# Performance work log

Hardware: AMD Instinct MI355X
Metric: run time of the kernel (lower is better)

The kernel has to match this reference:

```python
import jax, jax.numpy as jnp
import numpy as np

B, S, D, E, H, TOPK = 4, 2048, 1024, 32, 128, 4

def setup_inputs() -> dict:
    key = jax.random.key(0)
    k1, k2, k3, k4 = jax.random.split(key, 4)
    x = jax.random.normal(k1, (B, S, D), jnp.float32)
    expert_sel = jax.random.normal(k2, (E, D), jnp.float32) * (D ** -0.5)
    keys = jax.random.normal(k3, (E, D, H), jnp.float32) * (D ** -0.5)
    values = jax.random.normal(k4, (E, H, D), jnp.float32) * (H ** -0.5)
    return {"x": x, "expert_sel": expert_sel, "keys": keys, "values": values, "n_heads": TOPK}

def reference(x, expert_sel, keys, values, n_heads):
    # x: [B,S,D]; expert_sel: [E,D]; keys: [E,D,H]; values: [E,H,D]
    Bv, Sv, Dv = x.shape
    Ev = keys.shape[0]
    xf = x.reshape(-1, Dv)                                  # [N,D]
    N = xf.shape[0]
    gate = jax.nn.sigmoid(xf @ expert_sel.T)                # [N,E] sigmoid gating (sigma-MoE)
    vals, idx = jax.lax.top_k(gate, n_heads)                # [N,k] selected experts + gate weights
    # dense per-token-per-expert gate weights; zero for non-selected experts
    g = jnp.zeros((N, Ev), x.dtype).at[jnp.arange(N)[:, None], idx].set(vals)  # [N,E]
    # grouped expert FFN, expressed densely over the (small) expert axis:
    # out = sum_e g[n,e] * relu(x @ keys[e]) @ values[e]
    h = jax.nn.relu(jnp.einsum('nd,edh->enh', xf, keys))    # [E,N,H]
    out = jnp.einsum('enh,ehd->nd', h * g.T[:, :, None], values)  # [N,D]
    return out.reshape(Bv, Sv, Dv)
```

## Files before the change

kernel.cpp:

```cpp
#include <hip/hip_runtime.h>
#include <hip/hip_bf16.h>

#define NTOK 8192
#define DDIM 1024
#define NEXP 32
#define HDIM 128
#define TOPK 4

typedef __attribute__((ext_vector_type(8))) short bf16x8;
typedef __attribute__((ext_vector_type(4))) float f32x4;

typedef unsigned int uint_g __attribute__((address_space(1)));
typedef unsigned int uint_l __attribute__((address_space(3)));

__device__ __forceinline__ void async_cp16(const void* g, void* l) {
    __builtin_amdgcn_global_load_lds((const uint_g*)g, (uint_l*)l, 16, 0, 0);
}

__device__ inline unsigned short f2bf(float f) {
    unsigned int u = __builtin_bit_cast(unsigned int, f);
    unsigned int r = (u + 0x7fffu + ((u >> 16) & 1u)) >> 16;
    return (unsigned short)r;
}
__device__ inline float bf2f(unsigned short s) {
    unsigned int u = ((unsigned int)s) << 16;
    return __builtin_bit_cast(float, u);
}

__global__ __launch_bounds__(256) void prep_gate(
    const float* __restrict__ x, const float* __restrict__ es,
    const float* __restrict__ keys, const float* __restrict__ values,
    unsigned short* __restrict__ Kb, unsigned short* __restrict__ Vb,
    unsigned short* __restrict__ Xb,
    int* __restrict__ cnt, int* __restrict__ tok_list, float* __restrict__ gates)
{
    const int tid = threadIdx.x;

    if (blockIdx.x >= 512) {
        int idx = (int)(blockIdx.x - 512) * 256 + tid;
        unsigned short o[8];
        if (idx < NEXP * 128 * 128) {
            int n = idx & 127, k0 = (idx >> 7) & 127, e = idx >> 14;
            const float* s = keys + ((size_t)e * DDIM + k0 * 8) * HDIM + n;
            #pragma unroll
            for (int j = 0; j < 8; ++j) o[j] = f2bf(s[(size_t)j * HDIM]);
            *(uint4*)&Kb[(size_t)idx * 8] = *(uint4*)o;
        } else {
            idx -= NEXP * 128 * 128;
            int n = idx & 1023, k0 = (idx >> 10) & 15, e = idx >> 14;
            const float* s = values + ((size_t)e * HDIM + k0 * 8) * DDIM + n;
            #pragma unroll
            for (int j = 0; j < 8; ++j) o[j] = f2bf(s[(size_t)j * DDIM]);
            *(uint4*)&Vb[(size_t)idx * 8] = *(uint4*)o;
        }
        return;
    }

    const int n0 = (int)blockIdx.x * 16;

    __shared__ float smem[4608];
    __shared__ float Ls[16 * 33];
    __shared__ int hist[NEXP];
    __shared__ int bbase[NEXP];
    float* Xt  = smem;
    float* Est = smem + 64 * 36;
    float* Lp  = smem;

    const int t4  = (tid & 3) * 4;
    const int e4  = ((tid >> 2) & 7) * 4;
    const int rep = tid >> 5;

    const int xr = tid & 15, xc4 = (tid >> 4) * 4;
    const int er = tid & 31, ec8 = (tid >> 5) * 8;

    const int ctok = tid >> 4, cd4 = (tid & 15) * 4;

    const int rtok = tid >> 5, re = tid & 31;

    float lsum[2] = {0.f, 0.f};

    if (tid < NEXP) hist[tid] = 0;

    float4 xv  = *(const float4*)&x[(size_t)(n0 + xr) * DDIM + xc4];
    float4 ev0 = *(const float4*)&es[(size_t)er * DDIM + ec8];
    float4 ev1 = *(const float4*)&es[(size_t)er * DDIM + ec8 + 4];

    for (int q = 0; q < 4; ++q) {
        float acc[4][4] = {};

        for (int dci = 0; dci < 4; ++dci) {
            const int dc = q * 256 + dci * 64;
            __syncthreads();
            {
                Xt[(xc4 + 0) * 36 + xr] = xv.x; Xt[(xc4 + 1) * 36 + xr] = xv.y;
                Xt[(xc4 + 2) * 36 + xr] = xv.z; Xt[(xc4 + 3) * 36 + xr] = xv.w;
                Est[(ec8 + 0) * 36 + er] = ev0.x; Est[(ec8 + 1) * 36 + er] = ev0.y;
                Est[(ec8 + 2) * 36 + er] = ev0.z; Est[(ec8 + 3) * 36 + er] = ev0.w;
                Est[(ec8 + 4) * 36 + er] = ev1.x; Est[(ec8 + 5) * 36 + er] = ev1.y;
                Est[(ec8 + 6) * 36 + er] = ev1.z; Est[(ec8 + 7) * 36 + er] = ev1.w;
            }
            const int nxt = dc + 64;
            if (nxt < DDIM) {
                xv  = *(const float4*)&x[(size_t)(n0 + xr) * DDIM + nxt + xc4];
                ev0 = *(const float4*)&es[(size_t)er * DDIM + nxt + ec8];
                ev1 = *(const float4*)&es[(size_t)er * DDIM + nxt + ec8 + 4];
            }
            __syncthreads();

            {
                unsigned short o[4];
                #pragma unroll
                for (int j = 0; j < 4; ++j) o[j] = f2bf(Xt[(cd4 + j) * 36 + ctok]);
                *(uint2*)&Xb[(size_t)(n0 + ctok) * DDIM + dc + cd4] = *(uint2*)o;
            }

            #pragma unroll
            for (int s = 0; s < 8; ++s) {
                int d = s * 8 + rep;
                float4 xa4 = *(const float4*)&Xt[d * 36 + t4];
                float4 ea4 = *(const float4*)&Est[d * 36 + e4];
                const float xa[4] = {xa4.x, xa4.y, xa4.z, xa4.w};
                const float ea[4] = {ea4.x, ea4.y, ea4.z, ea4.w};
                #pragma unroll
                for (int i = 0; i < 4; ++i)
                    #pragma unroll
                    for (int j = 0; j < 4; ++j)
                        acc[i][j] = fmaf(xa[i], ea[j], acc[i][j]);
            }
        }

        __syncthreads();
        #pragma unroll
        for (int i = 0; i < 4; ++i)
            #pragma unroll
            for (int j = 0; j < 4; ++j)
                Lp[(rep * 16 + t4 + i) * 33 + e4 + j] = acc[i][j];
        __syncthreads();

        #pragma unroll
        for (int h = 0; h < 2; ++h) {
            int tok = rtok + h * 8;
            float s = 0.f;
            #pragma unroll
            for (int r = 0; r < 8; ++r) s += Lp[(r * 16 + tok) * 33 + re];
            lsum[h] += s;
        }
    }

    #pragma unroll
    for (int h = 0; h < 2; ++h) Ls[(rtok + h * 8) * 33 + re] = lsum[h];
    __syncthreads();

    int sel[TOPK]; int lpos[TOPK];
    if (tid < 16) {
        float lg[NEXP];
        #pragma unroll
        for (int e2 = 0; e2 < NEXP; ++e2) lg[e2] = Ls[tid * 33 + e2];
        float sv[TOPK];
        #pragma unroll
        for (int j = 0; j < TOPK; ++j) {
            float bv = -3.0e38f; int bi = 0;
            #pragma unroll
            for (int e2 = 0; e2 < NEXP; ++e2) {
                bool taken = false;
                #pragma unroll
                for (int qq = 0; qq < j; ++qq) taken = taken || (sel[qq] == e2);
                float v = taken ? -3.0e38f : lg[e2];
                if (v > bv) { bv = v; bi = e2; }
            }
            sel[j] = bi; sv[j] = bv;
        }
        #pragma unroll
        for (int j = 0; j < TOPK; ++j) {
            gates[(size_t)(n0 + tid) * TOPK + j] = 1.f / (1.f + expf(-sv[j]));
            lpos[j] = atomicAdd(&hist[sel[j]], 1);
        }
    }
    __syncthreads();
    if (tid < NEXP) bbase[tid] = atomicAdd(&cnt[tid], hist[tid]);
    __syncthreads();
    if (tid < 16) {
        #pragma unroll
        for (int j = 0; j < TOPK; ++j)
            tok_list[(size_t)sel[j] * NTOK + bbase[sel[j]] + lpos[j]] = (n0 + tid) * TOPK + j;
    }
}

__global__ __launch_bounds__(256) void ffn_fused(
    const unsigned short* __restrict__ Xb,
    const unsigned short* __restrict__ Kb,
    const unsigned short* __restrict__ Vb,
    const int* __restrict__ cnt, const int* __restrict__ tok_list,
    const float* __restrict__ gates,
    unsigned short* __restrict__ Ob)
{
    const int bid = blockIdx.x;
    const int e = bid & 31, tile = bid >> 5;
    const int c = cnt[e], base = tile * 64;
    if (base >= c) return;
    const int nt   = min(64, c - base);
    const int tid  = threadIdx.x, wave = tid >> 6, lane = tid & 63;
    const int lm   = lane & 15, quad = lane >> 4;
    const int r2   = (wave >> 1) * 32;
    const int c2   = (wave & 1) * 64;
    const int cw   = (wave & 1) * 32;

    __shared__ __align__(16) unsigned short KV[8192];
    __shared__ __align__(16) unsigned short XO[4608];
    __shared__ __align__(16) unsigned short Hs[64 * 140];
    __shared__ int slot[64]; __shared__ int gtok[64]; __shared__ float gs[64];

    if (tid < 64) {
        if (tid < nt) {
            int v = tok_list[(size_t)e * NTOK + base + tid];
            slot[tid] = v; gtok[tid] = v >> 2; gs[tid] = gates[v];
        } else { slot[tid] = -1; gtok[tid] = 0; gs[tid] = 0.f; }
    }
    __syncthreads();

    const unsigned short* Ke = Kb + (size_t)e * 131072;
    const unsigned short* Ve = Vb + (size_t)e * 131072;

    f32x4 acc[2][4];
    #pragma unroll
    for (int i = 0; i < 2; ++i)
        #pragma unroll
        for (int j = 0; j < 4; ++j) acc[i][j] = (f32x4){0.f, 0.f, 0.f, 0.f};

    const int xrow = (lane >> 3);
    const int xsub = (lane & 7);
    auto stageA = [&](int t) {
        int dc = t * 64;
        #pragma unroll
        for (int i = 0; i < 4; ++i) {
            int p = wave * 4 + i;
            async_cp16(Ke + ((size_t)(dc / 8 + (p >> 1)) * 128 + (p & 1) * 64 + lane) * 8,
                       &KV[p * 512]);
        }
        #pragma unroll
        for (int i = 0; i < 2; ++i) {
            int j = wave * 2 + i;
            int row = j * 8 + xrow;
            int u = xsub ^ (row & 7);
            async_cp16(Xb + (size_t)gtok[row] * DDIM + dc + u * 8, &XO[j * 512]);
        }
    };

    stageA(0);
    __syncthreads();

    const int xx = (quad << 3);
    for (int t = 0; t < 16; ++t) {
        #pragma unroll
        for (int ks = 0; ks < 2; ++ks) {
            int k0 = ks * 4 + quad;
            int xo = ((k0 ^ (lm & 7)) & 7) * 8;
            bf16x8 a0 = *(const bf16x8*)&XO[(r2 + lm) * 64 + xo];
            bf16x8 a1 = *(const bf16x8*)&XO[(r2 + 16 + lm) * 64 + xo];
            #pragma unroll
            for (int tj = 0; tj < 4; ++tj) {
                bf16x8 bb = *(const bf16x8*)&KV[(k0 * 128 + c2 + tj * 16 + lm) * 8];
                acc[0][tj] = __builtin_amdgcn_mfma_f32_16x16x32_bf16(a0, bb, acc[0][tj], 0, 0, 0);
                acc[1][tj] = __builtin_amdgcn_mfma_f32_16x16x32_bf16(a1, bb, acc[1][tj], 0, 0, 0);
            }
        }
        if (t < 15) {
            __syncthreads();
            stageA(t + 1);
            __syncthreads();
        }
    }
    (void)xx;

    #pragma unroll
    for (int ti = 0; ti < 2; ++ti)
        #pragma unroll
        for (int reg = 0; reg < 4; ++reg) {
            int m = r2 + ti * 16 + quad * 4 + reg;
            float g = gs[m];
            #pragma unroll
            for (int tj = 0; tj < 4; ++tj)
                Hs[m * 140 + c2 + tj * 16 + lm] = f2bf(fmaxf(acc[ti][tj][reg], 0.f) * g);
        }
    __syncthreads();

    auto stageV = [&](int cc) {
        #pragma unroll
        for (int i = 0; i < 4; ++i) {
            int p = wave * 4 + i;
            async_cp16(Ve + ((size_t)p * 1024 + cc * 64 + lane) * 8, &KV[p * 512]);
        }
    };

    stageV(0);

    bf16x8 hf[2][4];
    #pragma unroll
    for (int ks = 0; ks < 4; ++ks) {
        hf[0][ks] = *(const bf16x8*)&Hs[(r2 + lm) * 140 + (ks * 4 + quad) * 8];
        hf[1][ks] = *(const bf16x8*)&Hs[(r2 + 16 + lm) * 140 + (ks * 4 + quad) * 8];
    }
    __syncthreads();

    const int om = tid >> 2, oq = tid & 3;
    const int os = slot[om];

    for (int cc = 0; cc < 16; ++cc) {
        f32x4 acc2[2][2];
        #pragma unroll
        for (int i = 0; i < 2; ++i) {
            acc2[i][0] = (f32x4){0.f, 0.f, 0.f, 0.f};
            acc2[i][1] = (f32x4){0.f, 0.f, 0.f, 0.f};
        }

        #pragma unroll
        for (int ks = 0; ks < 4; ++ks) {
            int k0 = ks * 4 + quad;
            #pragma unroll
            for (int tj = 0; tj < 2; ++tj) {
                bf16x8 bb = *(const bf16x8*)&KV[(k0 * 64 + cw + tj * 16 + lm) * 8];
                acc2[0][tj] = __builtin_amdgcn_mfma_f32_16x16x32_bf16(hf[0][ks], bb, acc2[0][tj], 0, 0, 0);
                acc2[1][tj] = __builtin_amdgcn_mfma_f32_16x16x32_bf16(hf[1][ks], bb, acc2[1][tj], 0, 0, 0);
            }
        }

        #pragma unroll
        for (int ti = 0; ti < 2; ++ti)
            #pragma unroll
            for (int reg = 0; reg < 4; ++reg) {
                int m = r2 + ti * 16 + quad * 4 + reg;
                XO[m * 72 + cw + lm]      = f2bf(acc2[ti][0][reg]);
                XO[m * 72 + cw + 16 + lm] = f2bf(acc2[ti][1][reg]);
            }
        __syncthreads();

        if (os >= 0) {
            uint4 v0 = *(const uint4*)&XO[om * 72 + oq * 16];
            uint4 v1 = *(const uint4*)&XO[om * 72 + oq * 16 + 8];
            unsigned short* op = Ob + (size_t)os * DDIM + cc * 64 + oq * 16;
            *(uint4*)op       = v0;
            *(uint4*)(op + 8) = v1;
        }
        if (cc < 15) stageV(cc + 1);
        __syncthreads();
    }
}

__global__ __launch_bounds__(256) void reduce_out(
    const unsigned short* __restrict__ Ob, float* __restrict__ out)
{
    const int tid = threadIdx.x;
    const int n   = blockIdx.x * 2 + (tid >> 7);
    const int cc  = (tid & 127) * 8;

    float s[8] = {};
    #pragma unroll
    for (int j = 0; j < 4; ++j) {
        uint4 v = *(const uint4*)&Ob[((size_t)n * 4 + j) * DDIM + cc];
        const unsigned int w[4] = {v.x, v.y, v.z, v.w};
        #pragma unroll
        for (int q = 0; q < 4; ++q) {
            s[q * 2 + 0] += bf2f((unsigned short)(w[q] & 0xffff));
            s[q * 2 + 1] += bf2f((unsigned short)(w[q] >> 16));
        }
    }
    float4 o0 = {s[0], s[1], s[2], s[3]};
    float4 o1 = {s[4], s[5], s[6], s[7]};
    *(float4*)&out[(size_t)n * DDIM + cc]     = o0;
    *(float4*)&out[(size_t)n * DDIM + cc + 4] = o1;
}

extern "C" void kernel_launch(void* const* d_in, const int* in_sizes, int n_in,
                              void* d_out, int out_size, void* d_ws, size_t ws_size,
                              hipStream_t stream) {
    const float* x      = (const float*)d_in[0];
    const float* es     = (const float*)d_in[1];
    const float* keys   = (const float*)d_in[2];
    const float* values = (const float*)d_in[3];
    float* out          = (float*)d_out;

    char* w = (char*)d_ws;
    int*   cnt      = (int*)w;               w += 256;
    int*   tok_list = (int*)w;               w += (size_t)NEXP * NTOK * sizeof(int);
    float* gates    = (float*)w;             w += (size_t)NTOK * TOPK * sizeof(float);
    unsigned short* Kb = (unsigned short*)w; w += (size_t)NEXP * 128 * 128 * 8 * 2;
    unsigned short* Vb = (unsigned short*)w; w += (size_t)NEXP * 16 * 1024 * 8 * 2;
    unsigned short* Xb = (unsigned short*)w; w += (size_t)NTOK * DDIM * 2;
    unsigned short* Ob = (unsigned short*)w;

    hipMemsetAsync(cnt, 0, NEXP * sizeof(int), stream);

    prep_gate<<<512 + 4096, 256, 0, stream>>>(x, es, keys, values, Kb, Vb, Xb,
                                              cnt, tok_list, gates);
    ffn_fused<<<128 * NEXP, 256, 0, stream>>>(Xb, Kb, Vb, cnt, tok_list, gates, Ob);
    reduce_out<<<NTOK / 2, 256, 0, stream>>>(Ob, out);
}
```

Measured before the change: 186.3 us.

## Double-buffer K/X and V tiles in LDS to overlap async loads with MFMA

Merges the separate LDS arrays into one pool holding two buffers each for K/X tiles, V tiles and output staging. Tile t+2 is prefetched while tile t+1 is computed, and one barrier per iteration is dropped in both the up and down projection loops. The goal is to hide global-to-LDS latency behind MFMA work. The cost is more shared memory per block, which can lower the number of blocks resident per CU.

```diff
diff --git a/kernel.cpp b/kernel.cpp
--- a/kernel.cpp
+++ b/kernel.cpp
@@ -205,9 +205,7 @@
     const int c2   = (wave & 1) * 64;
     const int cw   = (wave & 1) * 32;
 
-    __shared__ __align__(16) unsigned short KV[8192];
-    __shared__ __align__(16) unsigned short XO[4608];
-    __shared__ __align__(16) unsigned short Hs[64 * 140];
+    __shared__ __align__(16) unsigned short P[34560];
     __shared__ int slot[64]; __shared__ int gtok[64]; __shared__ float gs[64];
 
     if (tid < 64) {
@@ -220,58 +218,67 @@
 
     const unsigned short* Ke = Kb + (size_t)e * 131072;
     const unsigned short* Ve = Vb + (size_t)e * 131072;
-
-    f32x4 acc[2][4];
-    #pragma unroll
-    for (int i = 0; i < 2; ++i)
-        #pragma unroll
-        for (int j = 0; j < 4; ++j) acc[i][j] = (f32x4){0.f, 0.f, 0.f, 0.f};
+    unsigned short* Hs = &P[25600];
 
     const int xrow = (lane >> 3);
     const int xsub = (lane & 7);
-    auto stageA = [&](int t) {
-        int dc = t * 64;
+    auto stageA = [&](int t, int cb) {
         #pragma unroll
         for (int i = 0; i < 4; ++i) {
             int p = wave * 4 + i;
-            async_cp16(Ke + ((size_t)(dc / 8 + (p >> 1)) * 128 + (p & 1) * 64 + lane) * 8,
-                       &KV[p * 512]);
+            async_cp16(Ke + ((size_t)(t * 8 + (p >> 1)) * 128 + (p & 1) * 64 + lane) * 8,
+                       &P[cb * 8192 + p * 512]);
         }
         #pragma unroll
         for (int i = 0; i < 2; ++i) {
             int j = wave * 2 + i;
             int row = j * 8 + xrow;
             int u = xsub ^ (row & 7);
-            async_cp16(Xb + (size_t)gtok[row] * DDIM + dc + u * 8, &XO[j * 512]);
+            async_cp16(Xb + (size_t)gtok[row] * DDIM + t * 64 + u * 8,
+                       &P[16384 + cb * 4096 + j * 512]);
         }
     };
-
-    stageA(0);
-    __syncthreads();
-
-    const int xx = (quad << 3);
+    auto stageV = [&](int cc, int vb) {
+        #pragma unroll
+        for (int i = 0; i < 4; ++i) {
+            int p = wave * 4 + i;
+            async_cp16(Ve + ((size_t)p * 1024 + cc * 64 + lane) * 8, &P[vb * 8192 + p * 512]);
+        }
+    };
+
+    f32x4 acc[2][4];
+    #pragma unroll
+    for (int i = 0; i < 2; ++i)
+        #pragma unroll
+        for (int j = 0; j < 4; ++j) acc[i][j] = (f32x4){0.f, 0.f, 0.f, 0.f};
+
+    stageA(0, 0);
+    stageA(1, 1);
+    __syncthreads();
+
     for (int t = 0; t < 16; ++t) {
+        const int cb = t & 1;
+        const unsigned short* KB_ = &P[cb * 8192];
+        const unsigned short* XB_ = &P[16384 + cb * 4096];
         #pragma unroll
         for (int ks = 0; ks < 2; ++ks) {
             int k0 = ks * 4 + quad;
             int xo = ((k0 ^ (lm & 7)) & 7) * 8;
-            bf16x8 a0 = *(const bf16x8*)&XO[(r2 + lm) * 64 + xo];
-            bf16x8 a1 = *(const bf16x8*)&XO[(r2 + 16 + lm) * 64 + xo];
+            bf16x8 a0 = *(const bf16x8*)&XB_[(r2 + lm) * 64 + xo];
+            bf16x8 a1 = *(const bf16x8*)&XB_[(r2 + 16 + lm) * 64 + xo];
             #pragma unroll
             for (int tj = 0; tj < 4; ++tj) {
-                bf16x8 bb = *(const bf16x8*)&KV[(k0 * 128 + c2 + tj * 16 + lm) * 8];
+                bf16x8 bb = *(const bf16x8*)&KB_[(k0 * 128 + c2 + tj * 16 + lm) * 8];
                 acc[0][tj] = __builtin_amdgcn_mfma_f32_16x16x32_bf16(a0, bb, acc[0][tj], 0, 0, 0);
                 acc[1][tj] = __builtin_amdgcn_mfma_f32_16x16x32_bf16(a1, bb, acc[1][tj], 0, 0, 0);
             }
         }
-        if (t < 15) {
-            __syncthreads();
-            stageA(t + 1);
-            __syncthreads();
-        }
-    }
-    (void)xx;
-
+        __syncthreads();
+        if (t + 2 < 16) stageA(t + 2, cb);
+    }
+
+    stageV(0, 0);
+    stageV(1, 1);
     #pragma unroll
     for (int ti = 0; ti < 2; ++ti)
         #pragma unroll
@@ -284,28 +291,21 @@
         }
     __syncthreads();
 
-    auto stageV = [&](int cc) {
-        #pragma unroll
-        for (int i = 0; i < 4; ++i) {
-            int p = wave * 4 + i;
-            async_cp16(Ve + ((size_t)p * 1024 + cc * 64 + lane) * 8, &KV[p * 512]);
-        }
-    };
-
-    stageV(0);
-
     bf16x8 hf[2][4];
     #pragma unroll
     for (int ks = 0; ks < 4; ++ks) {
         hf[0][ks] = *(const bf16x8*)&Hs[(r2 + lm) * 140 + (ks * 4 + quad) * 8];
         hf[1][ks] = *(const bf16x8*)&Hs[(r2 + 16 + lm) * 140 + (ks * 4 + quad) * 8];
     }
-    __syncthreads();
 
     const int om = tid >> 2, oq = tid & 3;
     const int os = slot[om];
 
     for (int cc = 0; cc < 16; ++cc) {
+        const int p = cc & 1;
+        const unsigned short* VB_ = &P[p * 8192];
+        unsigned short* OS_ = &P[16384 + p * 4608];
+
         f32x4 acc2[2][2];
         #pragma unroll
         for (int i = 0; i < 2; ++i) {
@@ -318,7 +318,7 @@
             int k0 = ks * 4 + quad;
             #pragma unroll
             for (int tj = 0; tj < 2; ++tj) {
-                bf16x8 bb = *(const bf16x8*)&KV[(k0 * 64 + cw + tj * 16 + lm) * 8];
+                bf16x8 bb = *(const bf16x8*)&VB_[(k0 * 64 + cw + tj * 16 + lm) * 8];
                 acc2[0][tj] = __builtin_amdgcn_mfma_f32_16x16x32_bf16(hf[0][ks], bb, acc2[0][tj], 0, 0, 0);
                 acc2[1][tj] = __builtin_amdgcn_mfma_f32_16x16x32_bf16(hf[1][ks], bb, acc2[1][tj], 0, 0, 0);
             }
@@ -329,20 +329,19 @@
             #pragma unroll
             for (int reg = 0; reg < 4; ++reg) {
                 int m = r2 + ti * 16 + quad * 4 + reg;
-                XO[m * 72 + cw + lm]      = f2bf(acc2[ti][0][reg]);
-                XO[m * 72 + cw + 16 + lm] = f2bf(acc2[ti][1][reg]);
+                OS_[m * 72 + cw + lm]      = f2bf(acc2[ti][0][reg]);
+                OS_[m * 72 + cw + 16 + lm] = f2bf(acc2[ti][1][reg]);
             }
         __syncthreads();
+        if (cc + 2 < 16) stageV(cc + 2, p);
 
         if (os >= 0) {
-            uint4 v0 = *(const uint4*)&XO[om * 72 + oq * 16];
-            uint4 v1 = *(const uint4*)&XO[om * 72 + oq * 16 + 8];
+            uint4 v0 = *(const uint4*)&OS_[om * 72 + oq * 16];
+            uint4 v1 = *(const uint4*)&OS_[om * 72 + oq * 16 + 8];
             unsigned short* op = Ob + (size_t)os * DDIM + cc * 64 + oq * 16;
             *(uint4*)op       = v0;
             *(uint4*)(op + 8) = v1;
         }
-        if (cc < 15) stageV(cc + 1);
-        __syncthreads();
     }
 }
 
```

After: 206.6 us. 10.9% more time.

## Fuse top-k output reduction into expert FFN via float atomic adds

Applied to the files above, without the earlier changes.

The expert FFN kernel no longer writes per-slot bf16 partial outputs that a separate reduce kernel sums. Each thread now atomically adds its fp32 accumulator values straight into the zero-initialized output, and the next V tile is staged before the atomics so the load overlaps them. This drops the Ob buffer round trip, the reduce launch and a bf16 rounding step. In exchange the kernel issues many scattered fp32 atomics (four contributions per output element), adds a full output memset, and makes the summation order nondeterministic.

```diff
diff --git a/kernel.cpp b/kernel.cpp
--- a/kernel.cpp
+++ b/kernel.cpp
@@ -21,10 +21,6 @@
     unsigned int u = __builtin_bit_cast(unsigned int, f);
     unsigned int r = (u + 0x7fffu + ((u >> 16) & 1u)) >> 16;
     return (unsigned short)r;
-}
-__device__ inline float bf2f(unsigned short s) {
-    unsigned int u = ((unsigned int)s) << 16;
-    return __builtin_bit_cast(float, u);
 }
 
 __global__ __launch_bounds__(256) void prep_gate(
@@ -192,7 +188,7 @@
     const unsigned short* __restrict__ Vb,
     const int* __restrict__ cnt, const int* __restrict__ tok_list,
     const float* __restrict__ gates,
-    unsigned short* __restrict__ Ob)
+    float* __restrict__ out)
 {
     const int bid = blockIdx.x;
     const int e = bid & 31, tile = bid >> 5;
@@ -206,7 +202,7 @@
     const int cw   = (wave & 1) * 32;
 
     __shared__ __align__(16) unsigned short KV[8192];
-    __shared__ __align__(16) unsigned short XO[4608];
+    __shared__ __align__(16) unsigned short XO[4096];
     __shared__ __align__(16) unsigned short Hs[64 * 140];
     __shared__ int slot[64]; __shared__ int gtok[64]; __shared__ float gs[64];
 
@@ -249,7 +245,6 @@
     stageA(0);
     __syncthreads();
 
-    const int xx = (quad << 3);
     for (int t = 0; t < 16; ++t) {
         #pragma unroll
         for (int ks = 0; ks < 2; ++ks) {
@@ -270,7 +265,6 @@
             __syncthreads();
         }
     }
-    (void)xx;
 
     #pragma unroll
     for (int ti = 0; ti < 2; ++ti)
@@ -300,10 +294,17 @@
         hf[0][ks] = *(const bf16x8*)&Hs[(r2 + lm) * 140 + (ks * 4 + quad) * 8];
         hf[1][ks] = *(const bf16x8*)&Hs[(r2 + 16 + lm) * 140 + (ks * 4 + quad) * 8];
     }
-    __syncthreads();
-
-    const int om = tid >> 2, oq = tid & 3;
-    const int os = slot[om];
+    int   trow[2][4];
+    bool  tval[2][4];
+    #pragma unroll
+    for (int ti = 0; ti < 2; ++ti)
+        #pragma unroll
+        for (int reg = 0; reg < 4; ++reg) {
+            int m = r2 + ti * 16 + quad * 4 + reg;
+            trow[ti][reg] = gtok[m];
+            tval[ti][reg] = (slot[m] >= 0);
+        }
+    __syncthreads();
 
     for (int cc = 0; cc < 16; ++cc) {
         f32x4 acc2[2][2];
@@ -323,51 +324,21 @@
                 acc2[1][tj] = __builtin_amdgcn_mfma_f32_16x16x32_bf16(hf[1][ks], bb, acc2[1][tj], 0, 0, 0);
             }
         }
+        __syncthreads();
+        if (cc < 15) stageV(cc + 1);
 
         #pragma unroll
         for (int ti = 0; ti < 2; ++ti)
             #pragma unroll
             for (int reg = 0; reg < 4; ++reg) {
-                int m = r2 + ti * 16 + quad * 4 + reg;
-                XO[m * 72 + cw + lm]      = f2bf(acc2[ti][0][reg]);
-                XO[m * 72 + cw + 16 + lm] = f2bf(acc2[ti][1][reg]);
+                if (tval[ti][reg]) {
+                    float* op = out + (size_t)trow[ti][reg] * DDIM + cc * 64 + cw + lm;
+                    unsafeAtomicAdd(op,      acc2[ti][0][reg]);
+                    unsafeAtomicAdd(op + 16, acc2[ti][1][reg]);
+                }
             }
         __syncthreads();
-
-        if (os >= 0) {
-            uint4 v0 = *(const uint4*)&XO[om * 72 + oq * 16];
-            uint4 v1 = *(const uint4*)&XO[om * 72 + oq * 16 + 8];
-            unsigned short* op = Ob + (size_t)os * DDIM + cc * 64 + oq * 16;
-            *(uint4*)op       = v0;
-            *(uint4*)(op + 8) = v1;
-        }
-        if (cc < 15) stageV(cc + 1);
-        __syncthreads();
-    }
-}
-
-__global__ __launch_bounds__(256) void reduce_out(
-    const unsigned short* __restrict__ Ob, float* __restrict__ out)
-{
-    const int tid = threadIdx.x;
-    const int n   = blockIdx.x * 2 + (tid >> 7);
-    const int cc  = (tid & 127) * 8;
-
-    float s[8] = {};
-    #pragma unroll
-    for (int j = 0; j < 4; ++j) {
-        uint4 v = *(const uint4*)&Ob[((size_t)n * 4 + j) * DDIM + cc];
-        const unsigned int w[4] = {v.x, v.y, v.z, v.w};
-        #pragma unroll
-        for (int q = 0; q < 4; ++q) {
-            s[q * 2 + 0] += bf2f((unsigned short)(w[q] & 0xffff));
-            s[q * 2 + 1] += bf2f((unsigned short)(w[q] >> 16));
-        }
-    }
-    float4 o0 = {s[0], s[1], s[2], s[3]};
-    float4 o1 = {s[4], s[5], s[6], s[7]};
-    *(float4*)&out[(size_t)n * DDIM + cc]     = o0;
-    *(float4*)&out[(size_t)n * DDIM + cc + 4] = o1;
+    }
 }
 
 extern "C" void kernel_launch(void* const* d_in, const int* in_sizes, int n_in,
@@ -386,12 +357,11 @@
     unsigned short* Kb = (unsigned short*)w; w += (size_t)NEXP * 128 * 128 * 8 * 2;
     unsigned short* Vb = (unsigned short*)w; w += (size_t)NEXP * 16 * 1024 * 8 * 2;
     unsigned short* Xb = (unsigned short*)w; w += (size_t)NTOK * DDIM * 2;
-    unsigned short* Ob = (unsigned short*)w;
 
     hipMemsetAsync(cnt, 0, NEXP * sizeof(int), stream);
+    hipMemsetAsync(out, 0, (size_t)NTOK * DDIM * sizeof(float), stream);
 
     prep_gate<<<512 + 4096, 256, 0, stream>>>(x, es, keys, values, Kb, Vb, Xb,
                                               cnt, tok_list, gates);
-    ffn_fused<<<128 * NEXP, 256, 0, stream>>>(Xb, Kb, Vb, cnt, tok_list, gates, Ob);
-    reduce_out<<<NTOK / 2, 256, 0, stream>>>(Ob, out);
-}
+    ffn_fused<<<128 * NEXP, 256, 0, stream>>>(Xb, Kb, Vb, cnt, tok_list, gates, out);
+}
```

Measured after the change: 266.2 us. +42.9%, slower.
